# Performance work log

Measured on AMD Instinct MI355X. Metric: run time of the kernel, lower is better.

## Reference

```python
import jax, jax.numpy as jnp
import numpy as np
from math import pi as PI

N = 50000      # nodes
E = 800000     # edges
G = 512        # graphs
L = 6          # num_layers
D = 128        # hidden_channels
F = 128        # num_filters
NG = 50        # num_gaussians
IN = 28        # input_dim
OUT = 32       # out_channels
CUT = 6.0      # cutoff
LN2 = float(np.log(2.0))
BN_EPS = 1e-5


def ssp(x):
    # ShiftedSoftplus
    return jax.nn.softplus(x) - LN2


def setup_inputs() -> dict:
    key = jax.random.key(0)
    ks = jax.random.split(key, 16)
    def rn(i, shape, s=0.05):
        return jax.random.normal(ks[i], shape, dtype=jnp.float32) * s
    return {
        "x": jax.random.normal(ks[0], (N, IN), dtype=jnp.float32),
        "pos": jax.random.normal(ks[1], (N, 3), dtype=jnp.float32) * 3.0,
        "batch": jnp.sort(jax.random.randint(ks[2], (N,), 0, G)),
        "edge_index": jax.random.randint(ks[3], (2, E), 0, N),
        # FeatureEmbedding: Linear(28,64) -> BN(64) -> ReLU -> Linear(64,128) -> ReLU
        "fe_w1": rn(4, (IN, D // 2)), "fe_b1": jnp.zeros((D // 2,), jnp.float32),
        "bn_gamma": jnp.ones((D // 2,), jnp.float32), "bn_beta": jnp.zeros((D // 2,), jnp.float32),
        "fe_w2": rn(5, (D // 2, D)), "fe_b2": jnp.zeros((D,), jnp.float32),
        # per-layer update_e: lin (no bias), mlp: Linear(NG,F)->SSP->Linear(F,F)
        "lin_w": rn(6, (L, D, F)),
        "mlp_w1": rn(7, (L, NG, F)), "mlp_b1": jnp.zeros((L, F), jnp.float32),
        "mlp_w2": rn(8, (L, F, F)), "mlp_b2": jnp.zeros((L, F), jnp.float32),
        # per-layer update_v: Linear(F,D)->SSP->Linear(D,D), residual
        "v1_w": rn(9, (L, F, D)), "v1_b": jnp.zeros((L, D), jnp.float32),
        "v2_w": rn(10, (L, D, D)), "v2_b": jnp.zeros((L, D), jnp.float32),
        # update_u: Linear(D,D//2)->SSP->Linear(D//2,OUT), then scatter over graphs
        "u1_w": rn(11, (D, D // 2)), "u1_b": jnp.zeros((D // 2,), jnp.float32),
        "u2_w": rn(12, (D // 2, OUT)), "u2_b": jnp.zeros((OUT,), jnp.float32),
    }


def reference(x, pos, batch, edge_index,
              fe_w1, fe_b1, bn_gamma, bn_beta, fe_w2, fe_b2,
              lin_w, mlp_w1, mlp_b1, mlp_w2, mlp_b2,
              v1_w, v1_b, v2_w, v2_b,
              u1_w, u1_b, u2_w, u2_b):
    row, col = edge_index[0], edge_index[1]  # (j, i): gather source j, scatter target i
    d = pos[row] - pos[col]                  # [E,3]
    dist = jnp.sqrt(jnp.sum(d * d, axis=-1))  # [E]
    offset = jnp.linspace(0.0, CUT, NG)
    coeff = -0.5 / (offset[1] - offset[0]) ** 2
    dist_emb = jnp.exp(coeff * (dist[:, None] - offset[None, :]) ** 2)  # [E,NG]
    cosC = 0.5 * (jnp.cos(dist * PI / CUT) + 1.0)                        # [E]

    # FeatureEmbedding (BatchNorm in training mode: batch statistics)
    h = x @ fe_w1 + fe_b1
    mu = jnp.mean(h, axis=0)
    var = jnp.mean((h - mu) ** 2, axis=0)
    h = (h - mu) / jnp.sqrt(var + BN_EPS) * bn_gamma + bn_beta
    h = jax.nn.relu(h)
    v = jax.nn.relu(h @ fe_w2 + fe_b2)  # [N,D]

    for l in range(L):
        # update_e: gate MLP on gaussian embedding, cosine cutoff, gather v[j]
        W = (ssp(dist_emb @ mlp_w1[l] + mlp_b1[l]) @ mlp_w2[l] + mlp_b2[l]) * cosC[:, None]  # [E,F]
        e = (v @ lin_w[l])[row] * W                                                          # [E,F]
        # update_v: scatter-add to nodes, MLP, residual
        agg = jax.ops.segment_sum(e, col, num_segments=N)                                    # [N,F]
        v = v + (ssp(agg @ v1_w[l] + v1_b[l]) @ v2_w[l] + v2_b[l])

    # update_u: per-node MLP then scatter-add per graph
    s = ssp(v @ u1_w + u1_b) @ u2_w + u2_b  # [N,OUT]
    return jax.ops.segment_sum(s, batch, num_segments=G)  # [G,OUT]
```

## Files before the change

kernel.cpp:

```cpp
#include <hip/hip_runtime.h>
#include <hip/hip_fp16.h>
#include <math.h>

#define DEV __device__ __forceinline__

constexpr int NGAUSS = 50;
constexpr int LAY = 6;
constexpr int K_TAB = 16384;
constexpr float DMAX = 40.0f;
constexpr float TSCALE = (float)(K_TAB - 1) / DMAX;
constexpr float STEP = 6.0f / 49.0f;
constexpr float COEFF = -0.5f / (STEP * STEP);
constexpr float LN2F = 0.69314718055994531f;
constexpr float PI_OVER_CUT = 0.52359877559829887f;

using f16x8 = __attribute__((ext_vector_type(8))) _Float16;
using f16x4 = __attribute__((ext_vector_type(4))) _Float16;
using f32x4 = __attribute__((ext_vector_type(4))) float;
using f32x8 = __attribute__((ext_vector_type(8))) float;

#define MFMA16(a, b, c) __builtin_amdgcn_mfma_f32_16x16x32_f16(a, b, c, 0, 0, 0)

DEV float sspf(float x) {
    float ax = fabsf(x);
    float e = __expf(-ax);
    return fmaxf(x, 0.f) + __logf(1.f + e) - LN2F;
}

DEV float4 ld_h4(const ushort* p) {
    uint2 r = *(const uint2*)p;
    __half2 a = __builtin_bit_cast(__half2, r.x);
    __half2 b = __builtin_bit_cast(__half2, r.y);
    float2 fa = __half22float2(a), fb = __half22float2(b);
    return make_float4(fa.x, fa.y, fb.x, fb.y);
}
DEV void st_h4(ushort* p, float4 v) {
    uint2 r;
    r.x = __builtin_bit_cast(uint, __float22half2_rn(make_float2(v.x, v.y)));
    r.y = __builtin_bit_cast(uint, __float22half2_rn(make_float2(v.z, v.w)));
    *(uint2*)p = r;
}

__global__ void k_cvtT128(const float* __restrict__ src, ushort* __restrict__ dst) {
    const float* s = src + (size_t)blockIdx.x * 16384;
    ushort* d = dst + (size_t)blockIdx.x * 16384;
    for (int i = threadIdx.x; i < 16384; i += 256) {
        int k = i >> 7, c = i & 127;
        d[(c << 7) + k] = __builtin_bit_cast(ushort, (_Float16)s[i]);
    }
}
__global__ void k_cvtT_fe(const float* __restrict__ src, ushort* __restrict__ dst) {
    for (int i = threadIdx.x; i < 8192; i += 256) {
        int k = i >> 7, c = i & 127;
        dst[(c << 6) + k] = __builtin_bit_cast(ushort, (_Float16)src[i]);
    }
}

__global__ void k_hist(const int* __restrict__ ei, int* __restrict__ counts, int E) {
    int e = blockIdx.x * 256 + threadIdx.x;
    if (e < E) atomicAdd(&counts[ei[E + e]], 1);
}

__global__ void k_scan1(const int* __restrict__ counts, int* __restrict__ locex,
                        int* __restrict__ bsum, int n) {
    __shared__ int s_wsum[16];
    const int tid = threadIdx.x;
    const int i = blockIdx.x * 1024 + tid;
    const int lane = tid & 63, wv = tid >> 6;
    int v = (i < n) ? counts[i] : 0;
    int x = v;
    #pragma unroll
    for (int off = 1; off < 64; off <<= 1) {
        int y = __shfl_up(x, off, 64);
        if (lane >= off) x += y;
    }
    if (lane == 63) s_wsum[wv] = x;
    __syncthreads();
    if (wv == 0 && lane < 16) {
        int wval = s_wsum[lane];
        int wx = wval;
        #pragma unroll
        for (int off = 1; off < 16; off <<= 1) {
            int wy = __shfl_up(wx, off, 16);
            if (lane >= off) wx += wy;
        }
        s_wsum[lane] = wx - wval;
    }
    __syncthreads();
    if (i < n) locex[i] = s_wsum[wv] + x - v;
    if (tid == 1023) bsum[blockIdx.x] = s_wsum[15] + x;
}

__global__ void k_scan2(int* __restrict__ bsum, int nb) {
    __shared__ int s_wsum[16];
    const int tid = threadIdx.x;
    const int lane = tid & 63, wv = tid >> 6;
    int v = (tid < nb) ? bsum[tid] : 0;
    int x = v;
    #pragma unroll
    for (int off = 1; off < 64; off <<= 1) {
        int y = __shfl_up(x, off, 64);
        if (lane >= off) x += y;
    }
    if (lane == 63) s_wsum[wv] = x;
    __syncthreads();
    if (wv == 0 && lane < 16) {
        int wval = s_wsum[lane];
        int wx = wval;
        #pragma unroll
        for (int off = 1; off < 16; off <<= 1) {
            int wy = __shfl_up(wx, off, 16);
            if (lane >= off) wx += wy;
        }
        s_wsum[lane] = wx - wval;
    }
    __syncthreads();
    if (tid < nb) bsum[tid] = s_wsum[wv] + x - v;
}

__global__ void k_scan3(const int* __restrict__ locex, const int* __restrict__ bsumex,
                        int* __restrict__ cursor, int* __restrict__ rowptr, int n) {
    int i = blockIdx.x * 256 + threadIdx.x;
    if (i >= n) return;
    int e = locex[i] + bsumex[i >> 10];
    cursor[i] = e;
    rowptr[i] = e;
}

__global__ void k_scatter(const int* __restrict__ ei, const float* __restrict__ pos,
                          int* __restrict__ cursor, uint* __restrict__ s_ef, int E) {
    int e = blockIdx.x * 256 + threadIdx.x;
    if (e >= E) return;
    int r = ei[e], c = ei[E + e];
    int p = atomicAdd(&cursor[c], 1);
    float dx = pos[3 * r + 0] - pos[3 * c + 0];
    float dy = pos[3 * r + 1] - pos[3 * c + 1];
    float dz = pos[3 * r + 2] - pos[3 * c + 2];
    float d = sqrtf(dx * dx + dy * dy + dz * dz);
    int i0 = (int)(d * TSCALE + 0.5f);
    if (i0 > K_TAB - 1) i0 = K_TAB - 1;
    s_ef[p] = (uint)r | ((uint)i0 << 16);
}

__launch_bounds__(256)
__global__ void k_tab_all(const float* __restrict__ w1A, const float* __restrict__ b1A,
                          const ushort* __restrict__ w2TA, const float* __restrict__ b2A,
                          ushort* __restrict__ tabA) {
    const int layer = blockIdx.x / (K_TAB / 32);
    const int k0 = (blockIdx.x % (K_TAB / 32)) * 32;
    const float* w1 = w1A + (size_t)layer * NGAUSS * 128;
    const float* b1 = b1A + (size_t)layer * 128;
    const ushort* w2T = w2TA + (size_t)layer * 16384;
    const float* b2 = b2A + (size_t)layer * 128;
    ushort* tab = tabA + (size_t)layer * K_TAB * 128;

    constexpr int LDP = 136;
    __shared__ float s_demb[32][NGAUSS];
    __shared__ _Float16 sT[32 * LDP];
    const int tid = threadIdx.x;

    for (int i = tid; i < 32 * NGAUSS; i += 256) {
        int r = i / NGAUSS, g = i - r * NGAUSS;
        float d = (float)(k0 + r) * (1.0f / TSCALE);
        float t = d - g * STEP;
        s_demb[r][g] = __expf(COEFF * t * t);
    }
    __syncthreads();

    {
        const int cg = tid & 31, rg = tid >> 5;
        const int r0 = rg << 2;
        const int c4 = cg << 2;
        float4 b1v = *(const float4*)&b1[c4];
        float4 acc[4];
        #pragma unroll
        for (int i = 0; i < 4; i++) acc[i] = b1v;
        #pragma unroll 2
        for (int k = 0; k < NGAUSS; k++) {
            float4 wv = *(const float4*)&w1[(k << 7) + c4];
            #pragma unroll
            for (int i = 0; i < 4; i++) {
                float dv = s_demb[r0 + i][k];
                acc[i].x = fmaf(dv, wv.x, acc[i].x);
                acc[i].y = fmaf(dv, wv.y, acc[i].y);
                acc[i].z = fmaf(dv, wv.z, acc[i].z);
                acc[i].w = fmaf(dv, wv.w, acc[i].w);
            }
        }
        #pragma unroll
        for (int i = 0; i < 4; i++) {
            f16x4 t;
            t[0] = (_Float16)sspf(acc[i].x);
            t[1] = (_Float16)sspf(acc[i].y);
            t[2] = (_Float16)sspf(acc[i].z);
            t[3] = (_Float16)sspf(acc[i].w);
            *(f16x4*)&sT[(r0 + i) * LDP + c4] = t;
        }
    }
    __syncthreads();

    const int wid = tid >> 6, lane = tid & 63;
    const int lr = lane & 15, lg = lane >> 4;
    const int kof = lg << 3;

    #pragma unroll
    for (int cb = 0; cb < 2; cb++) {
        const int col = ((2 * wid + cb) << 4) + lr;
        const ushort* bp = w2T + ((size_t)col << 7);
        f16x8 B0 = *(const f16x8*)(bp + kof);
        f16x8 B1 = *(const f16x8*)(bp + 32 + kof);
        f16x8 B2 = *(const f16x8*)(bp + 64 + kof);
        f16x8 B3 = *(const f16x8*)(bp + 96 + kof);
        float bb = b2[col];
        #pragma unroll
        for (int rt = 0; rt < 2; rt++) {
            const _Float16* ap = &sT[((rt << 4) + lr) * LDP + kof];
            f32x4 c = {0.f, 0.f, 0.f, 0.f};
            c = MFMA16(*(const f16x8*)ap, B0, c);
            c = MFMA16(*(const f16x8*)(ap + 32), B1, c);
            c = MFMA16(*(const f16x8*)(ap + 64), B2, c);
            c = MFMA16(*(const f16x8*)(ap + 96), B3, c);
            #pragma unroll
            for (int r = 0; r < 4; r++) {
                int knot = k0 + (rt << 4) + (lg << 2) + r;
                float d = (float)knot * (1.0f / TSCALE);
                float cc = 0.5f * (__cosf(d * PI_OVER_CUT) + 1.0f);
                tab[((size_t)knot << 7) + col] =
                    __builtin_bit_cast(ushort, (_Float16)((c[r] + bb) * cc));
            }
        }
    }
}

__launch_bounds__(256, 8)
__global__ void k_edge_csr(const uint* __restrict__ s_ef,
                           const int* __restrict__ rowptr, const int* __restrict__ counts,
                           const ushort* __restrict__ vlin, const ushort* __restrict__ tab,
                           ushort* __restrict__ agg, int N) {
    const int tid = threadIdx.x;
    const int l32 = tid & 31;
    const int h = l32 >> 4;
    const int lc = l32 & 15;
    const int n = blockIdx.x * 8 + (tid >> 5);
    if (n >= N) return;
    const ushort* tabc = tab + (lc << 3);
    const ushort* vlc  = vlin + (lc << 3);

    const int rs = rowptr[n];
    const int re = rs + counts[n];
    f32x8 acc = {0.f, 0.f, 0.f, 0.f, 0.f, 0.f, 0.f, 0.f};

    int e = rs + h;
    for (; e + 6 < re; e += 8) {
        f16x8 TP[4], VL[4];
        #pragma unroll
        for (int j = 0; j < 4; j++) {
            uint pk = s_ef[e + 2 * j];
            TP[j] = *(const f16x8*)(tabc + ((size_t)(pk >> 16) << 7));
            VL[j] = *(const f16x8*)(vlc + ((size_t)(pk & 0xFFFFu) << 7));
        }
        f16x8 p0 = TP[0] * VL[0];
        p0 += TP[1] * VL[1];
        f16x8 p1 = TP[2] * VL[2];
        p1 += TP[3] * VL[3];
        acc += __builtin_convertvector(p0, f32x8);
        acc += __builtin_convertvector(p1, f32x8);
    }
    for (; e < re; e += 2) {
        uint pk = s_ef[e];
        f16x8 tp = *(const f16x8*)(tabc + ((size_t)(pk >> 16) << 7));
        f16x8 vl = *(const f16x8*)(vlc + ((size_t)(pk & 0xFFFFu) << 7));
        acc += __builtin_convertvector(tp * vl, f32x8);
    }
    #pragma unroll
    for (int i = 0; i < 8; i++) acc[i] += __shfl_xor(acc[i], 16);
    if (h == 0) {
        f16x8 o;
        #pragma unroll
        for (int i = 0; i < 8; i++) o[i] = (_Float16)acc[i];
        *(f16x8*)&agg[((size_t)n << 7) + (lc << 3)] = o;
    }
}

__global__ void k_fe1(const float* __restrict__ x, const float* __restrict__ w,
                      const float* __restrict__ b, float* __restrict__ h, int N) {
    int idx = blockIdx.x * 256 + threadIdx.x;
    if (idx >= N * 64) return;
    int n = idx >> 6, c = idx & 63;
    const float* xr = x + (size_t)n * 28;
    float acc = b[c];
    #pragma unroll
    for (int k = 0; k < 28; k++) acc = fmaf(xr[k], w[k * 64 + c], acc);
    h[idx] = acc;
}

__global__ void k_bnstat(const float* __restrict__ h, float* __restrict__ stats, int N) {
    __shared__ float s_s[256], s_q[256];
    int tid = threadIdx.x;
    int c = tid & 63, g = tid >> 6;
    float s = 0.f, q = 0.f;
    for (int n = blockIdx.x * 4 + g; n < N; n += gridDim.x * 4) {
        float v = h[(size_t)n * 64 + c];
        s += v; q += v * v;
    }
    s_s[tid] = s; s_q[tid] = q;
    __syncthreads();
    if (tid < 64) {
        s = s_s[tid] + s_s[tid + 64] + s_s[tid + 128] + s_s[tid + 192];
        q = s_q[tid] + s_q[tid + 64] + s_q[tid + 128] + s_q[tid + 192];
        atomicAdd(&stats[tid], s);
        atomicAdd(&stats[64 + tid], q);
    }
}

__global__ void k_bnfin(const float* __restrict__ stats, float* __restrict__ prm,
                        const float* __restrict__ gamma, const float* __restrict__ beta,
                        float invN) {
    int c = threadIdx.x;
    float mu = stats[c] * invN;
    float var = stats[64 + c] * invN - mu * mu;
    float sc = gamma[c] * rsqrtf(var + 1e-5f);
    prm[c] = sc;
    prm[64 + c] = beta[c] - mu * sc;
}

__launch_bounds__(256, 4)
__global__ void k_fe2(const float* __restrict__ h, const float* __restrict__ prm,
                      const ushort* __restrict__ w2T, const float* __restrict__ b2,
                      ushort* __restrict__ v16, int N) {
    constexpr int LDP = 72;
    __shared__ _Float16 sH[64 * LDP];
    const int tid = threadIdx.x;
    const int n0 = blockIdx.x * 64;

    for (int i = tid; i < 64 * 16; i += 256) {
        int row = i >> 4, c4 = (i & 15) << 2;
        int gr = n0 + row;
        float4 hv = (gr < N) ? *(const float4*)&h[((size_t)gr << 6) + c4]
                             : make_float4(0.f, 0.f, 0.f, 0.f);
        float4 sc = *(const float4*)&prm[c4];
        float4 sh = *(const float4*)&prm[64 + c4];
        f16x4 o;
        o[0] = (_Float16)fmaxf(fmaf(hv.x, sc.x, sh.x), 0.f);
        o[1] = (_Float16)fmaxf(fmaf(hv.y, sc.y, sh.y), 0.f);
        o[2] = (_Float16)fmaxf(fmaf(hv.z, sc.z, sh.z), 0.f);
        o[3] = (_Float16)fmaxf(fmaf(hv.w, sc.w, sh.w), 0.f);
        *(f16x4*)&sH[row * LDP + c4] = o;
    }
    __syncthreads();

    const int wid = tid >> 6, lane = tid & 63;
    const int lr = lane & 15, lg = lane >> 4;
    const int kof = lg << 3;
    const int arow = wid * 16 + lr;
    const int drow0 = wid * 16 + (lg << 2);

    f16x8 a0 = *(const f16x8*)&sH[arow * LDP + kof];
    f16x8 a1 = *(const f16x8*)&sH[arow * LDP + 32 + kof];

    #pragma unroll
    for (int n = 0; n < 8; n++) {
        const ushort* bp = w2T + (((size_t)(n << 4) + lr) << 6);
        f32x4 c = {0.f, 0.f, 0.f, 0.f};
        c = MFMA16(a0, *(const f16x8*)(bp + kof), c);
        c = MFMA16(a1, *(const f16x8*)(bp + 32 + kof), c);
        int col = (n << 4) + lr;
        float bb = b2[col];
        #pragma unroll
        for (int r = 0; r < 4; r++) {
            int gr = n0 + drow0 + r;
            if (gr < N) v16[((size_t)gr << 7) + col] =
                __builtin_bit_cast(ushort, (_Float16)fmaxf(c[r] + bb, 0.f));
        }
    }
}

__launch_bounds__(256, 4)
__global__ void k_gemm_rb(const ushort* __restrict__ A, const ushort* __restrict__ wT,
                          ushort* __restrict__ C, int N) {
    constexpr int LDP = 136;
    __shared__ _Float16 sA[64 * LDP];
    const int tid = threadIdx.x;
    const int n0 = blockIdx.x * 64;

    for (int i = tid; i < 64 * 32; i += 256) {
        int row = i >> 5, c4 = (i & 31) << 2;
        int gr = n0 + row;
        uint2 val = (gr < N) ? *(const uint2*)&A[((size_t)gr << 7) + c4]
                             : make_uint2(0u, 0u);
        *(uint2*)&sA[row * LDP + c4] = val;
    }
    __syncthreads();

    const int wid = tid >> 6, lane = tid & 63;
    const int lr = lane & 15, lg = lane >> 4;
    const int kof = lg << 3;
    const int arow = wid * 16 + lr;
    const int drow0 = wid * 16 + (lg << 2);

    f16x8 a0 = *(const f16x8*)&sA[arow * LDP + kof];
    f16x8 a1 = *(const f16x8*)&sA[arow * LDP + 32 + kof];
    f16x8 a2 = *(const f16x8*)&sA[arow * LDP + 64 + kof];
    f16x8 a3 = *(const f16x8*)&sA[arow * LDP + 96 + kof];

    #pragma unroll
    for (int n = 0; n < 8; n++) {
        const ushort* bp = wT + (((size_t)(n << 4) + lr) << 7);
        f32x4 c = {0.f, 0.f, 0.f, 0.f};
        c = MFMA16(a0, *(const f16x8*)(bp + kof), c);
        c = MFMA16(a1, *(const f16x8*)(bp + 32 + kof), c);
        c = MFMA16(a2, *(const f16x8*)(bp + 64 + kof), c);
        c = MFMA16(a3, *(const f16x8*)(bp + 96 + kof), c);
        int col = (n << 4) + lr;
        #pragma unroll
        for (int r = 0; r < 4; r++) {
            int gr = n0 + drow0 + r;
            if (gr < N) C[((size_t)gr << 7) + col] =
                __builtin_bit_cast(ushort, (_Float16)c[r]);
        }
    }
}

__launch_bounds__(512, 8)
__global__ void k_update(const ushort* __restrict__ agg,
                         const ushort* __restrict__ w1T, const float* __restrict__ b1,
                         const ushort* __restrict__ w2T, const float* __restrict__ b2,
                         ushort* __restrict__ v16,
                         const ushort* __restrict__ linT, ushort* __restrict__ vlin, int N) {
    constexpr int LDP = 136;
    __shared__ _Float16 sA[64 * LDP];
    __shared__ _Float16 sB[64 * LDP];
    const int tid = threadIdx.x;
    const int n0 = blockIdx.x * 64;

    for (int i = tid; i < 64 * 32; i += 512) {
        int row = i >> 5, c4 = (i & 31) << 2;
        int gr = n0 + row;
        uint2 a = (gr < N) ? *(const uint2*)&agg[((size_t)gr << 7) + c4] : make_uint2(0u, 0u);
        uint2 b = (gr < N) ? *(const uint2*)&v16[((size_t)gr << 7) + c4] : make_uint2(0u, 0u);
        *(uint2*)&sA[row * LDP + c4] = a;
        *(uint2*)&sB[row * LDP + c4] = b;
    }
    __syncthreads();

    const int wid = tid >> 6, lane = tid & 63;
    const int lr = lane & 15, lg = lane >> 4;
    const int kof = lg << 3;
    const int col = (wid << 4) + lr;
    const int dr0 = lg << 2;

    f32x4 acc[4];

    {
        const ushort* bp = w1T + ((size_t)col << 7);
        f16x8 B0 = *(const f16x8*)(bp + kof);
        f16x8 B1 = *(const f16x8*)(bp + 32 + kof);
        f16x8 B2 = *(const f16x8*)(bp + 64 + kof);
        f16x8 B3 = *(const f16x8*)(bp + 96 + kof);
        #pragma unroll
        for (int rb = 0; rb < 4; rb++) {
            const _Float16* ap = &sA[((rb << 4) + lr) * LDP + kof];
            f32x4 c = {0.f, 0.f, 0.f, 0.f};
            c = MFMA16(*(const f16x8*)ap, B0, c);
            c = MFMA16(*(const f16x8*)(ap + 32), B1, c);
            c = MFMA16(*(const f16x8*)(ap + 64), B2, c);
            c = MFMA16(*(const f16x8*)(ap + 96), B3, c);
            acc[rb] = c;
        }
    }
    __syncthreads();
    {
        float bb = b1[col];
        #pragma unroll
        for (int rb = 0; rb < 4; rb++) {
            #pragma unroll
            for (int r = 0; r < 4; r++)
                sA[((rb << 4) + dr0 + r) * LDP + col] = (_Float16)sspf(acc[rb][r] + bb);
        }
    }
    __syncthreads();

    {
        const ushort* bp = w2T + ((size_t)col << 7);
        f16x8 B0 = *(const f16x8*)(bp + kof);
        f16x8 B1 = *(const f16x8*)(bp + 32 + kof);
        f16x8 B2 = *(const f16x8*)(bp + 64 + kof);
        f16x8 B3 = *(const f16x8*)(bp + 96 + kof);
        #pragma unroll
        for (int rb = 0; rb < 4; rb++) {
            const _Float16* ap = &sA[((rb << 4) + lr) * LDP + kof];
            f32x4 c = {0.f, 0.f, 0.f, 0.f};
            c = MFMA16(*(const f16x8*)ap, B0, c);
            c = MFMA16(*(const f16x8*)(ap + 32), B1, c);
            c = MFMA16(*(const f16x8*)(ap + 64), B2, c);
            c = MFMA16(*(const f16x8*)(ap + 96), B3, c);
            acc[rb] = c;
        }
    }
    {
        float bb = b2[col];
        #pragma unroll
        for (int rb = 0; rb < 4; rb++) {
            #pragma unroll
            for (int r = 0; r < 4; r++) {
                _Float16* p = &sB[((rb << 4) + dr0 + r) * LDP + col];
                *p = (_Float16)(acc[rb][r] + bb + (float)*p);
            }
        }
    }
    __syncthreads();

    for (int i = tid; i < 64 * 32; i += 512) {
        int row = i >> 5, c4 = (i & 31) << 2;
        int gr = n0 + row;
        if (gr < N) *(uint2*)&v16[((size_t)gr << 7) + c4] = *(const uint2*)&sB[row * LDP + c4];
    }
    if (!linT) return;

    {
        const ushort* bp = linT + ((size_t)col << 7);
        f16x8 B0 = *(const f16x8*)(bp + kof);
        f16x8 B1 = *(const f16x8*)(bp + 32 + kof);
        f16x8 B2 = *(const f16x8*)(bp + 64 + kof);
        f16x8 B3 = *(const f16x8*)(bp + 96 + kof);
        #pragma unroll
        for (int rb = 0; rb < 4; rb++) {
            const _Float16* ap = &sB[((rb << 4) + lr) * LDP + kof];
            f32x4 c = {0.f, 0.f, 0.f, 0.f};
            c = MFMA16(*(const f16x8*)ap, B0, c);
            c = MFMA16(*(const f16x8*)(ap + 32), B1, c);
            c = MFMA16(*(const f16x8*)(ap + 64), B2, c);
            c = MFMA16(*(const f16x8*)(ap + 96), B3, c);
            acc[rb] = c;
        }
    }
    #pragma unroll
    for (int rb = 0; rb < 4; rb++) {
        #pragma unroll
        for (int r = 0; r < 4; r++)
            sA[((rb << 4) + dr0 + r) * LDP + col] = (_Float16)acc[rb][r];
    }
    __syncthreads();

    for (int i = tid; i < 64 * 32; i += 512) {
        int row = i >> 5, c4 = (i & 31) << 2;
        int gr = n0 + row;
        if (gr < N) *(uint2*)&vlin[((size_t)gr << 7) + c4] = *(const uint2*)&sA[row * LDP + c4];
    }
}

__launch_bounds__(256, 4)
__global__ void k_uout(const ushort* __restrict__ v16, const float* __restrict__ u1w,
                       const float* __restrict__ u1b, const float* __restrict__ u2w,
                       const float* __restrict__ u2b, const int* __restrict__ batch,
                       float* __restrict__ out, int N) {
    __shared__ float sA[64 * 128];
    const int tid = threadIdx.x;
    const int n0 = blockIdx.x * 64;

    for (int i = tid; i < 64 * 32; i += 256) {
        int row = i >> 5, cq = (i & 31) << 2;
        int gr = n0 + row;
        float4 val = make_float4(0.f, 0.f, 0.f, 0.f);
        if (gr < N) val = ld_h4(&v16[((size_t)gr << 7) + cq]);
        *(float4*)&sA[row * 128 + cq] = val;
    }
    __syncthreads();

    const int cg = tid & 31, rg = tid >> 5;
    const int r0 = rg << 3;
    const int c2 = cg << 1;

    float2 acc[8];
    {
        float2 b1v = *(const float2*)&u1b[c2];
        #pragma unroll
        for (int i = 0; i < 8; i++) acc[i] = b1v;
        #pragma unroll 4
        for (int k = 0; k < 128; k++) {
            float2 wv = *(const float2*)&u1w[(k << 6) + c2];
            #pragma unroll
            for (int i = 0; i < 8; i++) {
                float a = sA[(r0 + i) * 128 + k];
                acc[i].x = fmaf(a, wv.x, acc[i].x);
                acc[i].y = fmaf(a, wv.y, acc[i].y);
            }
        }
    }
    __syncthreads();
    #pragma unroll
    for (int i = 0; i < 8; i++) {
        sA[(r0 + i) * 64 + c2 + 0] = sspf(acc[i].x);
        sA[(r0 + i) * 64 + c2 + 1] = sspf(acc[i].y);
    }
    __syncthreads();

    float acc2[8];
    {
        float bb = u2b[cg];
        #pragma unroll
        for (int i = 0; i < 8; i++) acc2[i] = bb;
        #pragma unroll 4
        for (int k = 0; k < 64; k++) {
            float wv = u2w[(k << 5) + cg];
            #pragma unroll
            for (int i = 0; i < 8; i++)
                acc2[i] = fmaf(sA[(r0 + i) * 64 + k], wv, acc2[i]);
        }
    }

    int cur = -1;
    float run = 0.f;
    #pragma unroll
    for (int i = 0; i < 8; i++) {
        int gr = n0 + r0 + i;
        int g = (gr < N) ? batch[gr] : -1;
        if (g != cur) {
            if (cur >= 0) atomicAdd(&out[(size_t)cur * 32 + cg], run);
            cur = g;
            run = 0.f;
        }
        if (g >= 0) run += acc2[i];
    }
    if (cur >= 0) atomicAdd(&out[(size_t)cur * 32 + cg], run);
}

extern "C" void kernel_launch(void* const* d_in, const int* in_sizes, int n_in,
                              void* d_out, int out_size, void* d_ws, size_t ws_size,
                              hipStream_t stream) {
    const float* x      = (const float*)d_in[0];
    const float* pos    = (const float*)d_in[1];
    const int*   batch  = (const int*)d_in[2];
    const int*   ei     = (const int*)d_in[3];
    const float* fe_w1  = (const float*)d_in[4];
    const float* fe_b1  = (const float*)d_in[5];
    const float* bn_g   = (const float*)d_in[6];
    const float* bn_b   = (const float*)d_in[7];
    const float* fe_w2  = (const float*)d_in[8];
    const float* fe_b2  = (const float*)d_in[9];
    const float* lin_w  = (const float*)d_in[10];
    const float* mlp_w1 = (const float*)d_in[11];
    const float* mlp_b1 = (const float*)d_in[12];
    const float* mlp_w2 = (const float*)d_in[13];
    const float* mlp_b2 = (const float*)d_in[14];
    const float* v1_w   = (const float*)d_in[15];
    const float* v1_b   = (const float*)d_in[16];
    const float* v2_w   = (const float*)d_in[17];
    const float* v2_b   = (const float*)d_in[18];
    const float* u1_w   = (const float*)d_in[19];
    const float* u1_b   = (const float*)d_in[20];
    const float* u2_w   = (const float*)d_in[21];
    const float* u2_b   = (const float*)d_in[22];

    const int N = in_sizes[0] / 28;
    const int E = in_sizes[3] / 2;
    const int NB1 = (N + 1023) / 1024;

    char* ws = (char*)d_ws;
    size_t o = 0;
    auto alloc = [&](size_t bytes) { void* p = ws + o; o += (bytes + 255) & ~(size_t)255; return p; };
    int*    counts = (int*)   alloc((size_t)N * 4);
    int*    cursor = (int*)   alloc((size_t)N * 4);
    int*    rowptr = (int*)   alloc((size_t)N * 4);
    int*    bsum   = (int*)   alloc((size_t)NB1 * 4);
    uint*   s_ef   = (uint*)  alloc((size_t)E * 4);
    float*  stats  = (float*) alloc(128 * 4);
    float*  prm    = (float*) alloc(128 * 4);
    ushort* tab    = (ushort*)alloc((size_t)LAY * K_TAB * 128 * 2);
    ushort* v16    = (ushort*)alloc((size_t)N * 128 * 2);
    ushort* vlin   = (ushort*)alloc((size_t)N * 128 * 2);
    ushort* agg    = (ushort*)alloc((size_t)N * 128 * 2);
    float*  h      = (float*) alloc((size_t)N * 64 * 4);
    int*    locex  = (int*)   alloc((size_t)N * 4);
    ushort* v1T    = (ushort*)alloc((size_t)LAY * 16384 * 2);
    ushort* v2T    = (ushort*)alloc((size_t)LAY * 16384 * 2);
    ushort* linT   = (ushort*)alloc((size_t)LAY * 16384 * 2);
    ushort* mw2T   = (ushort*)alloc((size_t)LAY * 16384 * 2);
    ushort* fe2T   = (ushort*)alloc((size_t)8192 * 2);

    k_cvtT128<<<LAY, 256, 0, stream>>>(v1_w, v1T);
    k_cvtT128<<<LAY, 256, 0, stream>>>(v2_w, v2T);
    k_cvtT128<<<LAY, 256, 0, stream>>>(lin_w, linT);
    k_cvtT128<<<LAY, 256, 0, stream>>>(mlp_w2, mw2T);
    k_cvtT_fe<<<1, 256, 0, stream>>>(fe_w2, fe2T);

    hipMemsetAsync(counts, 0, (size_t)N * 4, stream);
    k_hist<<<(E + 255) / 256, 256, 0, stream>>>(ei, counts, E);
    k_scan1<<<NB1, 1024, 0, stream>>>(counts, locex, bsum, N);
    k_scan2<<<1, 1024, 0, stream>>>(bsum, NB1);
    k_scan3<<<(N + 255) / 256, 256, 0, stream>>>(locex, bsum, cursor, rowptr, N);
    k_scatter<<<(E + 255) / 256, 256, 0, stream>>>(ei, pos, cursor, s_ef, E);

    k_tab_all<<<LAY * (K_TAB / 32), 256, 0, stream>>>(mlp_w1, mlp_b1, mw2T, mlp_b2, tab);

    hipMemsetAsync(stats, 0, 128 * 4, stream);
    k_fe1<<<(N * 64 + 255) / 256, 256, 0, stream>>>(x, fe_w1, fe_b1, h, N);
    k_bnstat<<<256, 256, 0, stream>>>(h, stats, N);
    k_bnfin<<<1, 64, 0, stream>>>(stats, prm, bn_g, bn_b, 1.0f / (float)N);
    const int gblk = (N + 63) / 64;
    k_fe2<<<gblk, 256, 0, stream>>>(h, prm, fe2T, fe_b2, v16, N);

    k_gemm_rb<<<gblk, 256, 0, stream>>>(v16, linT, vlin, N);

    const int eblk = (N + 7) / 8;
    for (int l = 0; l < LAY; l++) {
        k_edge_csr<<<eblk, 256, 0, stream>>>(
            s_ef, rowptr, counts, vlin,
            tab + (size_t)l * K_TAB * 128, agg, N);
        const ushort* lin_next = (l + 1 < LAY) ? linT + (size_t)(l + 1) * 16384 : nullptr;
        k_update<<<gblk, 512, 0, stream>>>(
            agg, v1T + (size_t)l * 16384, v1_b + (size_t)l * 128,
            v2T + (size_t)l * 16384, v2_b + (size_t)l * 128,
            v16, lin_next, vlin, N);
    }

    hipMemsetAsync(d_out, 0, (size_t)out_size * 4, stream);
    k_uout<<<gblk, 256, 0, stream>>>(v16, u1_w, u1_b, u2_w, u2_b, batch, (float*)d_out, N);
}
```

Before: 638.9 us.

## Halve distance table size and compute gate first layer with MFMA

Halves the number of knots in the per-layer distance lookup table, which halves table-build work and the table's memory footprint, making it more cache-friendly for the edge kernel's gathers. Moves the first gate MLP (gaussian embedding times w1) from scalar FP32 FMAs to fp16 MFMA, using a new transposed and zero-padded fp16 copy of mlp_w1. Precomputes the cosine cutoff once per knot into shared memory instead of once per output element. Risks lower accuracy from the coarser table interpolation and the fp16 embedding and weights.

```diff
diff --git a/kernel.cpp b/kernel.cpp
--- a/kernel.cpp
+++ b/kernel.cpp
@@ -6,7 +6,7 @@
 
 constexpr int NGAUSS = 50;
 constexpr int LAY = 6;
-constexpr int K_TAB = 16384;
+constexpr int K_TAB = 8192;
 constexpr float DMAX = 40.0f;
 constexpr float TSCALE = (float)(K_TAB - 1) / DMAX;
 constexpr float STEP = 6.0f / 49.0f;
@@ -34,12 +34,6 @@
     float2 fa = __half22float2(a), fb = __half22float2(b);
     return make_float4(fa.x, fa.y, fb.x, fb.y);
 }
-DEV void st_h4(ushort* p, float4 v) {
-    uint2 r;
-    r.x = __builtin_bit_cast(uint, __float22half2_rn(make_float2(v.x, v.y)));
-    r.y = __builtin_bit_cast(uint, __float22half2_rn(make_float2(v.z, v.w)));
-    *(uint2*)p = r;
-}
 
 __global__ void k_cvtT128(const float* __restrict__ src, ushort* __restrict__ dst) {
     const float* s = src + (size_t)blockIdx.x * 16384;
@@ -53,6 +47,15 @@
     for (int i = threadIdx.x; i < 8192; i += 256) {
         int k = i >> 7, c = i & 127;
         dst[(c << 6) + k] = __builtin_bit_cast(ushort, (_Float16)src[i]);
+    }
+}
+__global__ void k_cvtT_w1(const float* __restrict__ src, ushort* __restrict__ dst) {
+    const float* s = src + (size_t)blockIdx.x * (NGAUSS * 128);
+    ushort* d = dst + (size_t)blockIdx.x * (128 * 64);
+    for (int i = threadIdx.x; i < 128 * 64; i += 256) {
+        int c = i >> 6, k = i & 63;
+        float v = (k < NGAUSS) ? s[k * 128 + c] : 0.f;
+        d[(c << 6) + k] = __builtin_bit_cast(ushort, (_Float16)v);
     }
 }
 
@@ -143,65 +146,63 @@
 }
 
 __launch_bounds__(256)
-__global__ void k_tab_all(const float* __restrict__ w1A, const float* __restrict__ b1A,
+__global__ void k_tab_all(const ushort* __restrict__ w1TA, const float* __restrict__ b1A,
                           const ushort* __restrict__ w2TA, const float* __restrict__ b2A,
                           ushort* __restrict__ tabA) {
     const int layer = blockIdx.x / (K_TAB / 32);
     const int k0 = (blockIdx.x % (K_TAB / 32)) * 32;
-    const float* w1 = w1A + (size_t)layer * NGAUSS * 128;
+    const ushort* w1T = w1TA + (size_t)layer * 8192;
     const float* b1 = b1A + (size_t)layer * 128;
     const ushort* w2T = w2TA + (size_t)layer * 16384;
     const float* b2 = b2A + (size_t)layer * 128;
     ushort* tab = tabA + (size_t)layer * K_TAB * 128;
 
+    constexpr int LDD = 72;
     constexpr int LDP = 136;
-    __shared__ float s_demb[32][NGAUSS];
+    __shared__ _Float16 sD[32 * LDD];
     __shared__ _Float16 sT[32 * LDP];
+    __shared__ float s_cc[32];
     const int tid = threadIdx.x;
 
-    for (int i = tid; i < 32 * NGAUSS; i += 256) {
-        int r = i / NGAUSS, g = i - r * NGAUSS;
-        float d = (float)(k0 + r) * (1.0f / TSCALE);
-        float t = d - g * STEP;
-        s_demb[r][g] = __expf(COEFF * t * t);
-    }
-    __syncthreads();
-
-    {
-        const int cg = tid & 31, rg = tid >> 5;
-        const int r0 = rg << 2;
-        const int c4 = cg << 2;
-        float4 b1v = *(const float4*)&b1[c4];
-        float4 acc[4];
-        #pragma unroll
-        for (int i = 0; i < 4; i++) acc[i] = b1v;
-        #pragma unroll 2
-        for (int k = 0; k < NGAUSS; k++) {
-            float4 wv = *(const float4*)&w1[(k << 7) + c4];
-            #pragma unroll
-            for (int i = 0; i < 4; i++) {
-                float dv = s_demb[r0 + i][k];
-                acc[i].x = fmaf(dv, wv.x, acc[i].x);
-                acc[i].y = fmaf(dv, wv.y, acc[i].y);
-                acc[i].z = fmaf(dv, wv.z, acc[i].z);
-                acc[i].w = fmaf(dv, wv.w, acc[i].w);
-            }
-        }
-        #pragma unroll
-        for (int i = 0; i < 4; i++) {
-            f16x4 t;
-            t[0] = (_Float16)sspf(acc[i].x);
-            t[1] = (_Float16)sspf(acc[i].y);
-            t[2] = (_Float16)sspf(acc[i].z);
-            t[3] = (_Float16)sspf(acc[i].w);
-            *(f16x4*)&sT[(r0 + i) * LDP + c4] = t;
-        }
+    for (int i = tid; i < 32 * 64; i += 256) {
+        int r = i >> 6, g = i & 63;
+        float val = 0.f;
+        if (g < NGAUSS) {
+            float d = (float)(k0 + r) * (1.0f / TSCALE);
+            float t = d - g * STEP;
+            val = __expf(COEFF * t * t);
+        }
+        sD[r * LDD + g] = (_Float16)val;
+    }
+    if (tid < 32) {
+        float d = (float)(k0 + tid) * (1.0f / TSCALE);
+        s_cc[tid] = 0.5f * (__cosf(d * PI_OVER_CUT) + 1.0f);
     }
     __syncthreads();
 
     const int wid = tid >> 6, lane = tid & 63;
     const int lr = lane & 15, lg = lane >> 4;
     const int kof = lg << 3;
+
+    #pragma unroll
+    for (int cb = 0; cb < 2; cb++) {
+        const int col = ((2 * wid + cb) << 4) + lr;
+        const ushort* bp = w1T + ((size_t)col << 6);
+        f16x8 B0 = *(const f16x8*)(bp + kof);
+        f16x8 B1 = *(const f16x8*)(bp + 32 + kof);
+        float bb = b1[col];
+        #pragma unroll
+        for (int rt = 0; rt < 2; rt++) {
+            const _Float16* ap = &sD[((rt << 4) + lr) * LDD + kof];
+            f32x4 c = {0.f, 0.f, 0.f, 0.f};
+            c = MFMA16(*(const f16x8*)ap, B0, c);
+            c = MFMA16(*(const f16x8*)(ap + 32), B1, c);
+            #pragma unroll
+            for (int r = 0; r < 4; r++)
+                sT[((rt << 4) + (lg << 2) + r) * LDP + col] = (_Float16)sspf(c[r] + bb);
+        }
+    }
+    __syncthreads();
 
     #pragma unroll
     for (int cb = 0; cb < 2; cb++) {
@@ -222,11 +223,9 @@
             c = MFMA16(*(const f16x8*)(ap + 96), B3, c);
             #pragma unroll
             for (int r = 0; r < 4; r++) {
-                int knot = k0 + (rt << 4) + (lg << 2) + r;
-                float d = (float)knot * (1.0f / TSCALE);
-                float cc = 0.5f * (__cosf(d * PI_OVER_CUT) + 1.0f);
-                tab[((size_t)knot << 7) + col] =
-                    __builtin_bit_cast(ushort, (_Float16)((c[r] + bb) * cc));
+                int kr = (rt << 4) + (lg << 2) + r;
+                tab[((size_t)(k0 + kr) << 7) + col] =
+                    __builtin_bit_cast(ushort, (_Float16)((c[r] + bb) * s_cc[kr]));
             }
         }
     }
@@ -676,12 +675,14 @@
     ushort* v2T    = (ushort*)alloc((size_t)LAY * 16384 * 2);
     ushort* linT   = (ushort*)alloc((size_t)LAY * 16384 * 2);
     ushort* mw2T   = (ushort*)alloc((size_t)LAY * 16384 * 2);
+    ushort* mw1T   = (ushort*)alloc((size_t)LAY * 8192 * 2);
     ushort* fe2T   = (ushort*)alloc((size_t)8192 * 2);
 
     k_cvtT128<<<LAY, 256, 0, stream>>>(v1_w, v1T);
     k_cvtT128<<<LAY, 256, 0, stream>>>(v2_w, v2T);
     k_cvtT128<<<LAY, 256, 0, stream>>>(lin_w, linT);
     k_cvtT128<<<LAY, 256, 0, stream>>>(mlp_w2, mw2T);
+    k_cvtT_w1<<<LAY, 256, 0, stream>>>(mlp_w1, mw1T);
     k_cvtT_fe<<<1, 256, 0, stream>>>(fe_w2, fe2T);
 
     hipMemsetAsync(counts, 0, (size_t)N * 4, stream);
@@ -691,7 +692,7 @@
     k_scan3<<<(N + 255) / 256, 256, 0, stream>>>(locex, bsum, cursor, rowptr, N);
     k_scatter<<<(E + 255) / 256, 256, 0, stream>>>(ei, pos, cursor, s_ef, E);
 
-    k_tab_all<<<LAY * (K_TAB / 32), 256, 0, stream>>>(mlp_w1, mlp_b1, mw2T, mlp_b2, tab);
+    k_tab_all<<<LAY * (K_TAB / 32), 256, 0, stream>>>(mw1T, mlp_b1, mw2T, mlp_b2, tab);
 
     hipMemsetAsync(stats, 0, 128 * 4, stream);
     k_fe1<<<(N * 64 + 255) / 256, 256, 0, stream>>>(x, fe_w1, fe_b1, h, N);
```

New measurement: 601.4 us. 5.9% less time.
